# Performance work log

Hardware: AMD Instinct MI355X
Metric: run time of the kernel (lower is better)

Reference implementation:

```python
import jax, jax.numpy as jnp
import numpy as np

B, N, C = 8, 1024, 768
LOCAL_DIM = C // 2      # local_ratio = 0.5
GLOBAL_DIM = C - LOCAL_DIM
HEADS = 12 // 2         # num_heads // div
HEAD_DIM = GLOBAL_DIM // HEADS
SCALE = HEAD_DIM ** -0.5
KS = 3                  # local_ks
HIDDEN = 4 * C
EPS = 1e-6


def setup_inputs() -> dict:
    key = jax.random.key(0)
    ks = jax.random.split(key, 8)
    s = 0.02
    return {
        "x": jax.random.normal(ks[0], (B, N, C), jnp.float32),
        "ln1_g": jnp.ones((GLOBAL_DIM,), jnp.float32),
        "ln1_b": jnp.zeros((GLOBAL_DIM,), jnp.float32),
        "ln1l_g": jnp.ones((LOCAL_DIM,), jnp.float32),
        "ln1l_b": jnp.zeros((LOCAL_DIM,), jnp.float32),
        "g_qkv_w": jax.random.normal(ks[1], (GLOBAL_DIM, 3 * GLOBAL_DIM), jnp.float32) * s,
        "g_proj_w": jax.random.normal(ks[2], (GLOBAL_DIM, GLOBAL_DIM), jnp.float32) * s,
        "g_proj_b": jnp.zeros((GLOBAL_DIM,), jnp.float32),
        "l_qkv_w": jax.random.normal(ks[3], (LOCAL_DIM, 3 * LOCAL_DIM), jnp.float32) * s,
        "l_proj_w": jax.random.normal(ks[4], (LOCAL_DIM, LOCAL_DIM), jnp.float32) * s,
        "l_proj_b": jnp.zeros((LOCAL_DIM,), jnp.float32),
        "ln2_g": jnp.ones((C,), jnp.float32),
        "ln2_b": jnp.zeros((C,), jnp.float32),
        "fc1_w": jax.random.normal(ks[5], (C, HIDDEN), jnp.float32) * s,
        "fc1_b": jnp.zeros((HIDDEN,), jnp.float32),
        "fc2_w": jax.random.normal(ks[6], (HIDDEN, C), jnp.float32) * s,
        "fc2_b": jnp.zeros((C,), jnp.float32),
    }


def _ln(x, g, b):
    m = x.mean(-1, keepdims=True)
    v = x.var(-1, keepdims=True)  # biased, matches torch LayerNorm
    return (x - m) / jnp.sqrt(v + EPS) * g + b


def _mha(x, qkv_w, proj_w, proj_b, band=None):
    b, n, c = x.shape
    qkv = (x @ qkv_w).reshape(b, n, 3, HEADS, c // HEADS)
    q, k, v = qkv[:, :, 0], qkv[:, :, 1], qkv[:, :, 2]  # [b,n,h,d]
    scores = jnp.einsum('bnhd,bmhd->bhnm', q, k) * SCALE
    if band is not None:
        scores = jnp.where(band, scores, -jnp.inf)  # dense band mask, as in source
    a = jax.nn.softmax(scores, axis=-1)
    out = jnp.einsum('bhnm,bmhd->bnhd', a, v).reshape(b, n, c)
    return out @ proj_w + proj_b


def reference(x, ln1_g, ln1_b, ln1l_g, ln1l_b, g_qkv_w, g_proj_w, g_proj_b,
              l_qkv_w, l_proj_w, l_proj_b, ln2_g, ln2_b, fc1_w, fc1_b, fc2_w, fc2_b):
    idx = jnp.arange(N)
    # keep positions |i-j| <= ks//2 (clipping in the torch loop reduces to this band)
    band = (jnp.abs(idx[:, None] - idx[None, :]) <= KS // 2)[None, None]  # [1,1,N,N]
    xg = x[:, :, :GLOBAL_DIM]
    xl = x[:, :, GLOBAL_DIM:]
    attn_out = _mha(_ln(xg, ln1_g, ln1_b), g_qkv_w, g_proj_w, g_proj_b)
    local_out = _mha(_ln(xl, ln1l_g, ln1l_b), l_qkv_w, l_proj_w, l_proj_b, band=band)
    x = x + jnp.concatenate([attn_out, local_out], axis=-1)
    h = _ln(x, ln2_g, ln2_b)
    h = jax.nn.gelu(h @ fc1_w + fc1_b, approximate=False)  # torch default GELU is exact erf
    x = x + (h @ fc2_w + fc2_b)
    return x
```

## Files before the change

kernel.cpp:

```cpp
#include <hip/hip_runtime.h>

#define B_ 8
#define N_ 1024
#define C_ 768
#define H_ 6
#define HID_ 3072
#define EPSV 1e-6f
#define SCALE_V 0.125f
#define DPAD 70

typedef unsigned short u16t;
typedef unsigned int u32t;
typedef __attribute__((ext_vector_type(8))) short bf16x8;
typedef __attribute__((ext_vector_type(4))) float f32x4;

__device__ __forceinline__ float b2f(u16t u) {
  union { u32t i; float f; } c; c.i = ((u32t)u) << 16; return c.f;
}
__device__ __forceinline__ u16t f2b(float f) {
  union { float f; u32t i; } c; c.f = f;
  u32t r = c.i + 0x7FFFu + ((c.i >> 16) & 1u);
  return (u16t)(r >> 16);
}
__device__ __forceinline__ float ldval(const float* p) { return *p; }
__device__ __forceinline__ float ldval(const u16t* p) { return b2f(*p); }

__device__ __forceinline__ float gelu_f(float v) {
  const float u = v * (0.79788456f + 0.0356774081f * v * v);
  const float e = __expf(2.f * u);
  const float th = 1.f - 2.f / (e + 1.f);
  return 0.5f * v * (1.f + th);
}

__device__ __forceinline__ void gl16(const u16t* g, u16t* l) {
  __builtin_amdgcn_global_load_lds(
      (const __attribute__((address_space(1))) unsigned int*)g,
      (__attribute__((address_space(3))) unsigned int*)l, 16, 0, 0);
}

__device__ __forceinline__ int xcd_swz2() {
  const int gx = gridDim.x, gy = gridDim.y;
  const int nwg = gx * gy * gridDim.z;
  const int h = blockIdx.x + gx * (blockIdx.y + gy * blockIdx.z);
  const int nloc = nwg >> 3;
  const int rows = nloc / gx;
  const int xcd = h & 7;
  const int loc = h >> 3;
  const int bxl = loc / rows;
  const int byl = loc - bxl * rows;
  return xcd * nloc + byl * gx + bxl;
}

struct W6 {
  const float* w[6];
  u16t* wt[6];
  int K[6]; int N[6];
  int start[7];
};
__global__ __launch_bounds__(256) void prep_k(
    W6 d,
    const float* __restrict__ x,
    const float* __restrict__ gg, const float* __restrict__ gb,
    const float* __restrict__ lg, const float* __restrict__ lb,
    u16t* __restrict__ og, u16t* __restrict__ ol, int rows)
{
  __shared__ u16t tile[32][40];
  const int bid = blockIdx.x;
  if (bid < d.start[6]) {
    int z = 0;
    while (bid >= d.start[z + 1]) ++z;
    const float* W = d.w[z];
    u16t* Wt = d.wt[z];
    const int K = d.K[z], N = d.N[z];
    const int local = bid - d.start[z];
    const int nb = N >> 5;
    const int n0 = (local % nb) * 32, k0 = (local / nb) * 32;
    const int tx = threadIdx.x & 31, ty = threadIdx.x >> 5;
#pragma unroll
    for (int j = 0; j < 4; ++j) {
      const int k = ty + j * 8;
      tile[k][tx] = f2b(W[(size_t)(k0 + k) * N + n0 + tx]);
    }
    __syncthreads();
#pragma unroll
    for (int j = 0; j < 4; ++j) {
      const int n = ty + j * 8;
      Wt[(size_t)(n0 + n) * K + k0 + tx] = tile[tx][n];
    }
  } else {
    const int wv = threadIdx.x >> 6, lane = threadIdx.x & 63;
    const int row = (bid - d.start[6]) * 4 + wv;
    if (row >= rows) return;
    const float* ip = x + (size_t)row * 768;
    float xs[12];
    float s0 = 0.f, ss0 = 0.f, s1 = 0.f, ss1 = 0.f;
#pragma unroll
    for (int c = 0; c < 6; ++c) {
      float v = ip[c * 64 + lane];
      xs[c] = v; s0 += v; ss0 += v * v;
    }
#pragma unroll
    for (int c = 0; c < 6; ++c) {
      float v = ip[384 + c * 64 + lane];
      xs[6 + c] = v; s1 += v; ss1 += v * v;
    }
#pragma unroll
    for (int o = 32; o > 0; o >>= 1) {
      s0 += __shfl_xor(s0, o, 64); ss0 += __shfl_xor(ss0, o, 64);
      s1 += __shfl_xor(s1, o, 64); ss1 += __shfl_xor(ss1, o, 64);
    }
    const float m0 = s0 / 384.f, m1 = s1 / 384.f;
    const float i0 = 1.f / sqrtf(ss0 / 384.f - m0 * m0 + EPSV);
    const float i1 = 1.f / sqrtf(ss1 / 384.f - m1 * m1 + EPSV);
    u16t* o0 = og + (size_t)row * 384;
    u16t* o1 = ol + (size_t)row * 384;
#pragma unroll
    for (int c = 0; c < 6; ++c) {
      const int i = c * 64 + lane;
      o0[i] = f2b((xs[c] - m0) * i0 * gg[i] + gb[i]);
      o1[i] = f2b((xs[6 + c] - m1) * i1 * lg[i] + lb[i]);
    }
  }
}

__global__ __launch_bounds__(256) void ln2_vec(
    const u16t* __restrict__ in,
    const float* __restrict__ gam, const float* __restrict__ bet,
    u16t* __restrict__ outp, int rows)
{
  const int wv = threadIdx.x >> 6, lane = threadIdx.x & 63;
  const int row = blockIdx.x * 4 + wv;
  if (row >= rows) return;
  const u16t* ip = in + (size_t)row * 768;
  u16t va[8], vb[8];
  *reinterpret_cast<uint4*>(va) = *reinterpret_cast<const uint4*>(ip + lane * 8);
  const bool hasb = lane < 32;
  if (hasb)
    *reinterpret_cast<uint4*>(vb) = *reinterpret_cast<const uint4*>(ip + 512 + lane * 8);
  float xa[8], xb[8];
  float s = 0.f, ss = 0.f;
#pragma unroll
  for (int j = 0; j < 8; ++j) { xa[j] = b2f(va[j]); s += xa[j]; ss += xa[j] * xa[j]; }
  if (hasb) {
#pragma unroll
    for (int j = 0; j < 8; ++j) { xb[j] = b2f(vb[j]); s += xb[j]; ss += xb[j] * xb[j]; }
  }
#pragma unroll
  for (int o = 32; o > 0; o >>= 1) {
    s += __shfl_xor(s, o, 64);
    ss += __shfl_xor(ss, o, 64);
  }
  const float m = s / 768.f;
  const float inv = 1.f / sqrtf(ss / 768.f - m * m + EPSV);
  u16t* op = outp + (size_t)row * 768;
  {
    float4 g0 = *reinterpret_cast<const float4*>(gam + lane * 8);
    float4 g1 = *reinterpret_cast<const float4*>(gam + lane * 8 + 4);
    float4 b0 = *reinterpret_cast<const float4*>(bet + lane * 8);
    float4 b1 = *reinterpret_cast<const float4*>(bet + lane * 8 + 4);
    const float gg[8] = {g0.x, g0.y, g0.z, g0.w, g1.x, g1.y, g1.z, g1.w};
    const float bb[8] = {b0.x, b0.y, b0.z, b0.w, b1.x, b1.y, b1.z, b1.w};
    u16t ot[8];
#pragma unroll
    for (int j = 0; j < 8; ++j) ot[j] = f2b((xa[j] - m) * inv * gg[j] + bb[j]);
    *reinterpret_cast<uint4*>(op + lane * 8) = *reinterpret_cast<uint4*>(ot);
  }
  if (hasb) {
    float4 g0 = *reinterpret_cast<const float4*>(gam + 512 + lane * 8);
    float4 g1 = *reinterpret_cast<const float4*>(gam + 512 + lane * 8 + 4);
    float4 b0 = *reinterpret_cast<const float4*>(bet + 512 + lane * 8);
    float4 b1 = *reinterpret_cast<const float4*>(bet + 512 + lane * 8 + 4);
    const float gg[8] = {g0.x, g0.y, g0.z, g0.w, g1.x, g1.y, g1.z, g1.w};
    const float bb[8] = {b0.x, b0.y, b0.z, b0.w, b1.x, b1.y, b1.z, b1.w};
    u16t ot[8];
#pragma unroll
    for (int j = 0; j < 8; ++j) ot[j] = f2b((xb[j] - m) * inv * gg[j] + bb[j]);
    *reinterpret_cast<uint4*>(op + 512 + lane * 8) = *reinterpret_cast<uint4*>(ot);
  }
}

__global__ __launch_bounds__(256) void gemm_mfma(
    const u16t* __restrict__ A0, const u16t* __restrict__ A1, int lda,
    const u16t* __restrict__ B0, const u16t* __restrict__ B1, int ldb,
    const float* bias0, const float* bias1,
    const void* res0, const void* res1, int ldr, int res_f32,
    void* out0, void* out1, int ldo, int out_f32,
    int K, int act)
{
  __shared__ u16t pool[32768];
  u16t (*As)[64] = reinterpret_cast<u16t(*)[64]>(pool);
  u16t (*Bs)[64] = reinterpret_cast<u16t(*)[64]>(pool + 16384);
  const int gx = gridDim.x, gy = gridDim.y;
  int t0f = xcd_swz2();
  const int bx = t0f % gx;
  const int tmp = t0f / gx;
  const int by = tmp % gy;
  const int z = tmp / gy;

  const u16t* Aw  = z ? A1 : A0;
  const u16t* Btw = z ? B1 : B0;
  const float* bias = z ? bias1 : bias0;
  const void* res = z ? res1 : res0;
  void* outp = z ? out1 : out0;

  const int t = threadIdx.x;
  const int m0 = by * 128, n0 = bx * 128;
  const int wid = t >> 6, lane = t & 63;
  const int wr = wid >> 1, wc = wid & 1;
  const int lrow = lane & 15, lk = lane >> 4;

  const int srow = lane >> 3;
  const int scol = ((lane & 7) ^ srow) << 3;
  const u16t* aSrc = Aw  + (size_t)(m0 + wid * 32 + srow) * lda + scol;
  const u16t* bSrc = Btw + (size_t)(n0 + wid * 32 + srow) * ldb + scol;

  auto stage = [&](int bufi, int kt_) {
    u16t* aD = &As[bufi * 128 + wid * 32][0];
    u16t* bD = &Bs[bufi * 128 + wid * 32][0];
#pragma unroll
    for (int i = 0; i < 4; ++i) {
      gl16(aSrc + (size_t)i * 8 * lda + kt_ * 64, aD + i * 8 * 64);
      gl16(bSrc + (size_t)i * 8 * ldb + kt_ * 64, bD + i * 8 * 64);
    }
  };

  f32x4 acc[4][4];
#pragma unroll
  for (int m = 0; m < 4; ++m)
#pragma unroll
    for (int n = 0; n < 4; ++n) acc[m][n] = (f32x4)(0.f);

  const int nt = K >> 6;
  stage(0, 0);
  for (int kt = 0; kt < nt; ++kt) {
    const int cur = kt & 1;
    if (kt + 1 < nt) {
      stage(cur ^ 1, kt + 1);
      asm volatile("s_waitcnt vmcnt(8)" ::: "memory");
    } else {
      asm volatile("s_waitcnt vmcnt(0)" ::: "memory");
    }
    __builtin_amdgcn_s_barrier();
    __builtin_amdgcn_sched_barrier(0);
#pragma unroll
    for (int kk = 0; kk < 2; ++kk) {
      bf16x8 aF[4], bF[4];
      const int k8 = kk * 4 + lk;
#pragma unroll
      for (int f = 0; f < 4; ++f) {
        const int ar = wr * 64 + f * 16 + lrow;
        aF[f] = *reinterpret_cast<const bf16x8*>(&As[cur * 128 + ar][(k8 ^ (ar & 7)) << 3]);
        const int br = wc * 64 + f * 16 + lrow;
        bF[f] = *reinterpret_cast<const bf16x8*>(&Bs[cur * 128 + br][(k8 ^ (br & 7)) << 3]);
      }
#pragma unroll
      for (int m = 0; m < 4; ++m)
#pragma unroll
        for (int n = 0; n < 4; ++n)
          acc[m][n] = __builtin_amdgcn_mfma_f32_16x16x32_bf16(
              aF[m], bF[n], acc[m][n], 0, 0, 0);
    }
    __builtin_amdgcn_s_barrier();
  }

  const int orow0 = (lane >> 4) * 4;
  const int ocol = lane & 15;
  if (out_f32) {
    float (*Cf)[128] = reinterpret_cast<float(*)[128]>(pool);
    __syncthreads();
#pragma unroll
    for (int m = 0; m < 4; ++m) {
#pragma unroll
      for (int n = 0; n < 4; ++n) {
        const int lc2 = wc * 64 + n * 16 + ocol;
        const int gn = n0 + lc2;
        const float bv = bias ? bias[gn] : 0.f;
#pragma unroll
        for (int i = 0; i < 4; ++i) {
          const int lr = wr * 64 + m * 16 + orow0 + i;
          float v = acc[m][n][i] + bv;
          if (act == 1) v = gelu_f(v);
          if (res) v += res_f32 ? ((const float*)res)[(size_t)(m0 + lr) * ldr + gn]
                                : b2f(((const u16t*)res)[(size_t)(m0 + lr) * ldr + gn]);
          Cf[lr][lc2] = v;
        }
      }
    }
    __syncthreads();
    float* ou = (float*)outp;
#pragma unroll
    for (int j = 0; j < 16; ++j) {
      const int c = j * 256 + t;
      const int r = c >> 5, ch = (c & 31) * 4;
      *reinterpret_cast<float4*>(ou + (size_t)(m0 + r) * ldo + n0 + ch) =
          *reinterpret_cast<const float4*>(&Cf[r][ch]);
    }
  } else {
    u16t (*Cs)[136] = reinterpret_cast<u16t(*)[136]>(pool);
    __syncthreads();
#pragma unroll
    for (int m = 0; m < 4; ++m) {
#pragma unroll
      for (int n = 0; n < 4; ++n) {
        const int lc2 = wc * 64 + n * 16 + ocol;
        const int gn = n0 + lc2;
        const float bv = bias ? bias[gn] : 0.f;
#pragma unroll
        for (int i = 0; i < 4; ++i) {
          const int lr = wr * 64 + m * 16 + orow0 + i;
          float v = acc[m][n][i] + bv;
          if (act == 1) v = gelu_f(v);
          if (res) v += res_f32 ? ((const float*)res)[(size_t)(m0 + lr) * ldr + gn]
                                : b2f(((const u16t*)res)[(size_t)(m0 + lr) * ldr + gn]);
          Cs[lr][lc2] = f2b(v);
        }
      }
    }
    __syncthreads();
    u16t* ou = (u16t*)outp;
#pragma unroll
    for (int j = 0; j < 8; ++j) {
      const int c = j * 256 + t;
      const int r = c >> 4, ch = (c & 15) * 8;
      *reinterpret_cast<uint4*>(ou + (size_t)(m0 + r) * ldo + n0 + ch) =
          *reinterpret_cast<const uint4*>(&Cs[r][ch]);
    }
  }
}

__global__ __launch_bounds__(256) void gemm64_drain(
    const u16t* __restrict__ A, int lda,
    const u16t* __restrict__ Bt, int ldb,
    const float* __restrict__ bias,
    const void* __restrict__ res, int ldr, int res_f32,
    void* __restrict__ outp, int ldo, int out_f32,
    int K, int act)
{
  __shared__ u16t pool[16384];
  u16t (*As)[64] = reinterpret_cast<u16t(*)[64]>(pool);
  u16t (*Bs)[64] = reinterpret_cast<u16t(*)[64]>(pool + 4096);
  const int gx = gridDim.x, gy = gridDim.y;
  int t0f = xcd_swz2();
  const int bx = t0f % gx;
  const int by = (t0f / gx) % gy;

  const int t = threadIdx.x;
  const int m0 = by * 64, n0 = bx * 128;
  const int wid = t >> 6, lane = t & 63;
  const int wr = wid >> 1, wc = wid & 1;
  const int lrow = lane & 15, lk = lane >> 4;

  const int srow = lane >> 3;
  const int scol = ((lane & 7) ^ srow) << 3;
  const u16t* aSrc = A  + (size_t)(m0 + wid * 16 + srow) * lda + scol;
  const u16t* bSrc = Bt + (size_t)(n0 + wid * 32 + srow) * ldb + scol;

  f32x4 acc[2][4];
#pragma unroll
  for (int m = 0; m < 2; ++m)
#pragma unroll
    for (int n = 0; n < 4; ++n) acc[m][n] = (f32x4)(0.f);

  const int nt = K >> 6;
  for (int kt = 0; kt < nt; ++kt) {
    {
      u16t* aD = &As[wid * 16][0];
      u16t* bD = &Bs[wid * 32][0];
#pragma unroll
      for (int i = 0; i < 2; ++i)
        gl16(aSrc + (size_t)i * 8 * lda + kt * 64, aD + i * 8 * 64);
#pragma unroll
      for (int i = 0; i < 4; ++i)
        gl16(bSrc + (size_t)i * 8 * ldb + kt * 64, bD + i * 8 * 64);
    }
    asm volatile("s_waitcnt vmcnt(0)" ::: "memory");
    __builtin_amdgcn_s_barrier();
    __builtin_amdgcn_sched_barrier(0);
#pragma unroll
    for (int kk = 0; kk < 2; ++kk) {
      bf16x8 aF[2], bF[4];
      const int k8 = kk * 4 + lk;
#pragma unroll
      for (int f = 0; f < 2; ++f) {
        const int ar = wr * 32 + f * 16 + lrow;
        aF[f] = *reinterpret_cast<const bf16x8*>(&As[ar][(k8 ^ (ar & 7)) << 3]);
      }
#pragma unroll
      for (int f = 0; f < 4; ++f) {
        const int br = wc * 64 + f * 16 + lrow;
        bF[f] = *reinterpret_cast<const bf16x8*>(&Bs[br][(k8 ^ (br & 7)) << 3]);
      }
#pragma unroll
      for (int m = 0; m < 2; ++m)
#pragma unroll
        for (int n = 0; n < 4; ++n)
          acc[m][n] = __builtin_amdgcn_mfma_f32_16x16x32_bf16(
              aF[m], bF[n], acc[m][n], 0, 0, 0);
    }
    __builtin_amdgcn_s_barrier();
  }

  const int orow0 = (lane >> 4) * 4;
  const int ocol = lane & 15;
  if (out_f32) {
    float (*Cf)[128] = reinterpret_cast<float(*)[128]>(pool);
    __syncthreads();
#pragma unroll
    for (int m = 0; m < 2; ++m) {
#pragma unroll
      for (int n = 0; n < 4; ++n) {
        const int lc2 = wc * 64 + n * 16 + ocol;
        const int gn = n0 + lc2;
        const float bv = bias ? bias[gn] : 0.f;
#pragma unroll
        for (int i = 0; i < 4; ++i) {
          const int lr = wr * 32 + m * 16 + orow0 + i;
          float v = acc[m][n][i] + bv;
          if (act == 1) v = gelu_f(v);
          if (res) v += res_f32 ? ((const float*)res)[(size_t)(m0 + lr) * ldr + gn]
                                : b2f(((const u16t*)res)[(size_t)(m0 + lr) * ldr + gn]);
          Cf[lr][lc2] = v;
        }
      }
    }
    __syncthreads();
    float* ou = (float*)outp;
#pragma unroll
    for (int j = 0; j < 8; ++j) {
      const int c = j * 256 + t;
      const int r = c >> 5, ch = (c & 31) * 4;
      *reinterpret_cast<float4*>(ou + (size_t)(m0 + r) * ldo + n0 + ch) =
          *reinterpret_cast<const float4*>(&Cf[r][ch]);
    }
  } else {
    u16t (*Cs)[136] = reinterpret_cast<u16t(*)[136]>(pool);
    __syncthreads();
#pragma unroll
    for (int m = 0; m < 2; ++m) {
#pragma unroll
      for (int n = 0; n < 4; ++n) {
        const int lc2 = wc * 64 + n * 16 + ocol;
        const int gn = n0 + lc2;
        const float bv = bias ? bias[gn] : 0.f;
#pragma unroll
        for (int i = 0; i < 4; ++i) {
          const int lr = wr * 32 + m * 16 + orow0 + i;
          float v = acc[m][n][i] + bv;
          if (act == 1) v = gelu_f(v);
          if (res) v += res_f32 ? ((const float*)res)[(size_t)(m0 + lr) * ldr + gn]
                                : b2f(((const u16t*)res)[(size_t)(m0 + lr) * ldr + gn]);
          Cs[lr][lc2] = f2b(v);
        }
      }
    }
    __syncthreads();
    u16t* ou = (u16t*)outp;
#pragma unroll
    for (int j = 0; j < 4; ++j) {
      const int c = j * 256 + t;
      const int r = c >> 4, ch = (c & 15) * 8;
      *reinterpret_cast<uint4*>(ou + (size_t)(m0 + r) * ldo + n0 + ch) =
          *reinterpret_cast<const uint4*>(&Cs[r][ch]);
    }
  }
}

__global__ __launch_bounds__(256) void attn_both(
    const u16t* __restrict__ qkvg, const u16t* __restrict__ qkvl,
    u16t* __restrict__ og, u16t* __restrict__ ol)
{
  __shared__ u16t Ks[64][DPAD];
  __shared__ u16t Vt[64][DPAD];
  __shared__ u16t Pw[4][16][DPAD];
  const int t = threadIdx.x;
  const int bid = blockIdx.x;

  if (bid < 768) {
    const int tf = (bid & 7) * 96 + (bid >> 3);
    const int q0 = (tf % 16) * 64;
    const int h = (tf / 16) % H_;
    const int b = tf / (16 * H_);
    const size_t base = (size_t)b * N_ * 1152 + h * 64;

    const int wid = t >> 6, lane = t & 63;
    const int lc = lane & 15;
    const int lg = lane >> 4;

    bf16x8 qf[2];
    {
      const u16t* qp = qkvg + base + (size_t)(q0 + wid * 16 + lc) * 1152 + 8 * lg;
      qf[0] = *reinterpret_cast<const bf16x8*>(qp);
      qf[1] = *reinterpret_cast<const bf16x8*>(qp + 32);
    }

    f32x4 Of[4];
#pragma unroll
    for (int nf = 0; nf < 4; ++nf) Of[nf] = (f32x4)(0.f);
    float m_run[4], l_run[4];
#pragma unroll
    for (int i = 0; i < 4; ++i) { m_run[i] = -INFINITY; l_run[i] = 0.f; }

    const int sj = t >> 2, sd0 = (t & 3) * 16;

    for (int kt = 0; kt < 16; ++kt) {
      __syncthreads();
      {
        const u16t* kp = qkvg + base + (size_t)(kt * 64 + sj) * 1152 + 384 + sd0;
        uint4 k0 = *reinterpret_cast<const uint4*>(kp);
        uint4 k1 = *reinterpret_cast<const uint4*>(kp + 8);
        *reinterpret_cast<uint4*>(&Ks[sj][sd0])     = k0;
        *reinterpret_cast<uint4*>(&Ks[sj][sd0 + 8]) = k1;
        const u16t* vp = kp + 384;
        u16t tv[16];
        *reinterpret_cast<uint4*>(tv)     = *reinterpret_cast<const uint4*>(vp);
        *reinterpret_cast<uint4*>(tv + 8) = *reinterpret_cast<const uint4*>(vp + 8);
#pragma unroll
        for (int e = 0; e < 16; ++e) Vt[sd0 + e][sj] = tv[e];
      }
      __syncthreads();

      f32x4 sc[4];
#pragma unroll
      for (int nf = 0; nf < 4; ++nf) sc[nf] = (f32x4)(0.f);
      __builtin_amdgcn_s_setprio(1);
#pragma unroll
      for (int kc = 0; kc < 2; ++kc) {
#pragma unroll
        for (int nf = 0; nf < 4; ++nf) {
          bf16x8 kf = *reinterpret_cast<const bf16x8*>(&Ks[nf * 16 + lc][8 * lg + 32 * kc]);
          sc[nf] = __builtin_amdgcn_mfma_f32_16x16x32_bf16(qf[kc], kf, sc[nf], 0, 0, 0);
        }
      }
      __builtin_amdgcn_s_setprio(0);

#pragma unroll
      for (int i = 0; i < 4; ++i) {
        float s0 = sc[0][i] * SCALE_V, s1 = sc[1][i] * SCALE_V;
        float s2 = sc[2][i] * SCALE_V, s3 = sc[3][i] * SCALE_V;
        float mi = fmaxf(fmaxf(s0, s1), fmaxf(s2, s3));
#pragma unroll
        for (int o = 8; o > 0; o >>= 1) mi = fmaxf(mi, __shfl_xor(mi, o, 64));
        const float nm = fmaxf(m_run[i], mi);
        const float alpha = __expf(m_run[i] - nm);
        m_run[i] = nm;
        float p0 = __expf(s0 - nm), p1 = __expf(s1 - nm);
        float p2 = __expf(s2 - nm), p3 = __expf(s3 - nm);
        const int prow = lg * 4 + i;
        Pw[wid][prow][lc]      = f2b(p0);
        Pw[wid][prow][16 + lc] = f2b(p1);
        Pw[wid][prow][32 + lc] = f2b(p2);
        Pw[wid][prow][48 + lc] = f2b(p3);
        float ls = p0 + p1 + p2 + p3;
#pragma unroll
        for (int o = 8; o > 0; o >>= 1) ls += __shfl_xor(ls, o, 64);
        l_run[i] = l_run[i] * alpha + ls;
#pragma unroll
        for (int nf = 0; nf < 4; ++nf) Of[nf][i] *= alpha;
      }

      __builtin_amdgcn_s_setprio(1);
#pragma unroll
      for (int kc = 0; kc < 2; ++kc) {
        bf16x8 pf = *reinterpret_cast<const bf16x8*>(&Pw[wid][lc][8 * lg + 32 * kc]);
#pragma unroll
        for (int nf = 0; nf < 4; ++nf) {
          bf16x8 vf = *reinterpret_cast<const bf16x8*>(&Vt[nf * 16 + lc][8 * lg + 32 * kc]);
          Of[nf] = __builtin_amdgcn_mfma_f32_16x16x32_bf16(pf, vf, Of[nf], 0, 0, 0);
        }
      }
      __builtin_amdgcn_s_setprio(0);
    }

#pragma unroll
    for (int i = 0; i < 4; ++i) {
      const float inv = 1.f / l_run[i];
      const size_t row = (size_t)b * N_ + q0 + wid * 16 + lg * 4 + i;
#pragma unroll
      for (int nf = 0; nf < 4; ++nf)
        og[row * 384 + h * 64 + nf * 16 + lc] = f2b(Of[nf][i] * inv);
    }
  } else {
    const int tg = (bid - 768) * 256 + t;
    const int h = tg % H_;
    const int n = (tg / H_) % N_;
    const int b = tg / (H_ * N_);
    const size_t qb = ((size_t)b * N_ + n) * 1152 + h * 64;

    float q[64];
#pragma unroll
    for (int dc = 0; dc < 8; ++dc) {
      u16t tq[8];
      *reinterpret_cast<uint4*>(tq) = *reinterpret_cast<const uint4*>(qkvl + qb + dc * 8);
#pragma unroll
      for (int s2 = 0; s2 < 8; ++s2) q[dc * 8 + s2] = b2f(tq[s2]);
    }

    const int jm = (n > 0) ? n - 1 : 0;
    const int jp = (n < N_ - 1) ? n + 1 : N_ - 1;
    const size_t kb0 = ((size_t)b * N_ + jm) * 1152 + 384 + h * 64;
    const size_t kb1 = ((size_t)b * N_ + n ) * 1152 + 384 + h * 64;
    const size_t kb2 = ((size_t)b * N_ + jp) * 1152 + 384 + h * 64;

    float s0 = 0.f, s1 = 0.f, s2v = 0.f;
#pragma unroll
    for (int dc = 0; dc < 8; ++dc) {
      u16t t0[8], t1[8], t2[8];
      *reinterpret_cast<uint4*>(t0) = *reinterpret_cast<const uint4*>(qkvl + kb0 + dc * 8);
      *reinterpret_cast<uint4*>(t1) = *reinterpret_cast<const uint4*>(qkvl + kb1 + dc * 8);
      *reinterpret_cast<uint4*>(t2) = *reinterpret_cast<const uint4*>(qkvl + kb2 + dc * 8);
#pragma unroll
      for (int s = 0; s < 8; ++s) {
        float qv = q[dc * 8 + s];
        s0 = fmaf(qv, b2f(t0[s]), s0);
        s1 = fmaf(qv, b2f(t1[s]), s1);
        s2v = fmaf(qv, b2f(t2[s]), s2v);
      }
    }
    s0 = (n > 0)      ? s0 * SCALE_V : -1e30f;
    s1 = s1 * SCALE_V;
    s2v = (n < N_ - 1) ? s2v * SCALE_V : -1e30f;
    float m = fmaxf(s1, fmaxf(s0, s2v));
    float p0 = __expf(s0 - m), p1 = __expf(s1 - m), p2 = __expf(s2v - m);
    float inv = 1.f / (p0 + p1 + p2);
    p0 *= inv; p1 *= inv; p2 *= inv;

    const size_t vb0 = kb0 + 384, vb1 = kb1 + 384, vb2 = kb2 + 384;
    u16t* op = ol + ((size_t)b * N_ + n) * 384 + h * 64;
#pragma unroll
    for (int dc = 0; dc < 8; ++dc) {
      u16t t0[8], t1[8], t2[8], ot[8];
      *reinterpret_cast<uint4*>(t0) = *reinterpret_cast<const uint4*>(qkvl + vb0 + dc * 8);
      *reinterpret_cast<uint4*>(t1) = *reinterpret_cast<const uint4*>(qkvl + vb1 + dc * 8);
      *reinterpret_cast<uint4*>(t2) = *reinterpret_cast<const uint4*>(qkvl + vb2 + dc * 8);
#pragma unroll
      for (int s = 0; s < 8; ++s)
        ot[s] = f2b(p0 * b2f(t0[s]) + p1 * b2f(t1[s]) + p2 * b2f(t2[s]));
      *reinterpret_cast<uint4*>(op + dc * 8) = *reinterpret_cast<uint4*>(ot);
    }
  }
}

extern "C" void kernel_launch(void* const* d_in, const int* in_sizes, int n_in,
                              void* d_out, int out_size, void* d_ws, size_t ws_size,
                              hipStream_t stream) {
  const float* x        = (const float*)d_in[0];
  const float* ln1_g    = (const float*)d_in[1];
  const float* ln1_b    = (const float*)d_in[2];
  const float* ln1l_g   = (const float*)d_in[3];
  const float* ln1l_b   = (const float*)d_in[4];
  const float* g_qkv_w  = (const float*)d_in[5];
  const float* g_proj_w = (const float*)d_in[6];
  const float* g_proj_b = (const float*)d_in[7];
  const float* l_qkv_w  = (const float*)d_in[8];
  const float* l_proj_w = (const float*)d_in[9];
  const float* l_proj_b = (const float*)d_in[10];
  const float* ln2_g    = (const float*)d_in[11];
  const float* ln2_b    = (const float*)d_in[12];
  const float* fc1_w    = (const float*)d_in[13];
  const float* fc1_b    = (const float*)d_in[14];
  const float* fc2_w    = (const float*)d_in[15];
  const float* fc2_b    = (const float*)d_in[16];
  float* out = (float*)d_out;
  u16t* ws = (u16t*)d_ws;

  u16t* gqkv_wt = ws + 0;
  u16t* lqkv_wt = ws + 442368;
  u16t* gproj_wt= ws + 884736;
  u16t* lproj_wt= ws + 1032192;
  u16t* fc1_wt  = ws + 1179648;
  u16t* fc2_wt  = ws + 3538944;
  u16t* lng  = ws + 5898240;
  u16t* lnl  = ws + 9043968;
  u16t* qkvg = ws + 12189696;
  u16t* qkvl = ws + 21626880;
  u16t* attg = lng;
  u16t* attl = lnl;
  u16t* x1   = ws + 12189696;
  u16t* ln2o = ws + 5898240;
  u16t* hbuf = ws + 18481152;

  const int rows = B_ * N_;

  W6 w6;
  w6.w[0] = g_qkv_w;  w6.wt[0] = gqkv_wt;  w6.K[0] = 384;  w6.N[0] = 1152;
  w6.w[1] = l_qkv_w;  w6.wt[1] = lqkv_wt;  w6.K[1] = 384;  w6.N[1] = 1152;
  w6.w[2] = g_proj_w; w6.wt[2] = gproj_wt; w6.K[2] = 384;  w6.N[2] = 384;
  w6.w[3] = l_proj_w; w6.wt[3] = lproj_wt; w6.K[3] = 384;  w6.N[3] = 384;
  w6.w[4] = fc1_w;    w6.wt[4] = fc1_wt;   w6.K[4] = 768;  w6.N[4] = 3072;
  w6.w[5] = fc2_w;    w6.wt[5] = fc2_wt;   w6.K[5] = 3072; w6.N[5] = 768;
  int acc0 = 0;
  for (int i = 0; i < 6; ++i) {
    w6.start[i] = acc0;
    acc0 += (w6.N[i] / 32) * (w6.K[i] / 32);
  }
  w6.start[6] = acc0;

  prep_k<<<dim3(acc0 + 2048), 256, 0, stream>>>(
      w6, x, ln1_g, ln1_b, ln1l_g, ln1l_b, lng, lnl, rows);

  gemm_mfma<<<dim3(9, 64, 2), 256, 0, stream>>>(
      lng, lnl, 384, gqkv_wt, lqkv_wt, 384,
      nullptr, nullptr, nullptr, nullptr, 0, 0,
      qkvg, qkvl, 1152, 0, 384, 0);

  attn_both<<<dim3(960), 256, 0, stream>>>(qkvg, qkvl, attg, attl);

  gemm_mfma<<<dim3(3, 64, 2), 256, 0, stream>>>(
      attg, attl, 384, gproj_wt, lproj_wt, 384,
      g_proj_b, l_proj_b, x, x + 384, 768, 1,
      x1, x1 + 384, 768, 0, 384, 0);

  ln2_vec<<<dim3(2048), 256, 0, stream>>>(x1, ln2_g, ln2_b, ln2o, rows);

  gemm_mfma<<<dim3(24, 64, 1), 256, 0, stream>>>(
      ln2o, ln2o, 768, fc1_wt, fc1_wt, 768,
      fc1_b, fc1_b, nullptr, nullptr, 0, 0,
      hbuf, hbuf, 3072, 0, 768, 1);

  gemm64_drain<<<dim3(6, 128), 256, 0, stream>>>(
      hbuf, 3072, fc2_wt, 3072, fc2_b, x1, 768, 0,
      out, 768, 1, 3072, 0);
}
```

Before: 255.6 us.

## Use 64-row single-buffer GEMM for QKV/proj, specialize FC1 kernel

Drops the double-buffered 128x128 generic GEMM. The QKV and projection GEMMs now run through the 64x128 single-buffer drain kernel, extended to take two batched z-slices, which doubles the block count and uses less LDS per block. FC1 gets its own 128x128 single-buffer kernel with bias and GELU hard-coded and half the shared memory. This aims at better occupancy and tail behaviour, but gives up the overlap of global loads with MFMA compute.

Measured after the change: 232.4 us (median of 2 runs). 1.1x faster.

```diff
diff --git a/kernel.cpp b/kernel.cpp
--- a/kernel.cpp
+++ b/kernel.cpp
@@ -179,161 +179,105 @@
   }
 }
 
-__global__ __launch_bounds__(256) void gemm_mfma(
+__global__ __launch_bounds__(256) void gemm128_fc1(
+    const u16t* __restrict__ A, int lda,
+    const u16t* __restrict__ Bt, int ldb,
+    const float* __restrict__ bias,
+    u16t* __restrict__ outp, int ldo, int K)
+{
+  __shared__ u16t pool[17408];
+  u16t (*As)[64] = reinterpret_cast<u16t(*)[64]>(pool);
+  u16t (*Bs)[64] = reinterpret_cast<u16t(*)[64]>(pool + 8192);
+  const int gx = gridDim.x, gy = gridDim.y;
+  int t0f = xcd_swz2();
+  const int bx = t0f % gx;
+  const int by = (t0f / gx) % gy;
+
+  const int t = threadIdx.x;
+  const int m0 = by * 128, n0 = bx * 128;
+  const int wid = t >> 6, lane = t & 63;
+  const int wr = wid >> 1, wc = wid & 1;
+  const int lrow = lane & 15, lk = lane >> 4;
+
+  const int srow = lane >> 3;
+  const int scol = ((lane & 7) ^ srow) << 3;
+  const u16t* aSrc = A  + (size_t)(m0 + wid * 32 + srow) * lda + scol;
+  const u16t* bSrc = Bt + (size_t)(n0 + wid * 32 + srow) * ldb + scol;
+
+  f32x4 acc[4][4];
+#pragma unroll
+  for (int m = 0; m < 4; ++m)
+#pragma unroll
+    for (int n = 0; n < 4; ++n) acc[m][n] = (f32x4)(0.f);
+
+  const int nt = K >> 6;
+  for (int kt = 0; kt < nt; ++kt) {
+    {
+      u16t* aD = &As[wid * 32][0];
+      u16t* bD = &Bs[wid * 32][0];
+#pragma unroll
+      for (int i = 0; i < 4; ++i) {
+        gl16(aSrc + (size_t)i * 8 * lda + kt * 64, aD + i * 8 * 64);
+        gl16(bSrc + (size_t)i * 8 * ldb + kt * 64, bD + i * 8 * 64);
+      }
+    }
+    asm volatile("s_waitcnt vmcnt(0)" ::: "memory");
+    __builtin_amdgcn_s_barrier();
+    __builtin_amdgcn_sched_barrier(0);
+#pragma unroll
+    for (int kk = 0; kk < 2; ++kk) {
+      bf16x8 aF[4], bF[4];
+      const int k8 = kk * 4 + lk;
+#pragma unroll
+      for (int f = 0; f < 4; ++f) {
+        const int ar = wr * 64 + f * 16 + lrow;
+        aF[f] = *reinterpret_cast<const bf16x8*>(&As[ar][(k8 ^ (ar & 7)) << 3]);
+        const int br = wc * 64 + f * 16 + lrow;
+        bF[f] = *reinterpret_cast<const bf16x8*>(&Bs[br][(k8 ^ (br & 7)) << 3]);
+      }
+#pragma unroll
+      for (int m = 0; m < 4; ++m)
+#pragma unroll
+        for (int n = 0; n < 4; ++n)
+          acc[m][n] = __builtin_amdgcn_mfma_f32_16x16x32_bf16(
+              aF[m], bF[n], acc[m][n], 0, 0, 0);
+    }
+    __builtin_amdgcn_s_barrier();
+  }
+
+  const int orow0 = (lane >> 4) * 4;
+  const int ocol = lane & 15;
+  u16t (*Cs)[136] = reinterpret_cast<u16t(*)[136]>(pool);
+  __syncthreads();
+#pragma unroll
+  for (int m = 0; m < 4; ++m) {
+#pragma unroll
+    for (int n = 0; n < 4; ++n) {
+      const int lc2 = wc * 64 + n * 16 + ocol;
+      const float bv = bias[n0 + lc2];
+#pragma unroll
+      for (int i = 0; i < 4; ++i) {
+        const int lr = wr * 64 + m * 16 + orow0 + i;
+        Cs[lr][lc2] = f2b(gelu_f(acc[m][n][i] + bv));
+      }
+    }
+  }
+  __syncthreads();
+#pragma unroll
+  for (int j = 0; j < 8; ++j) {
+    const int c = j * 256 + t;
+    const int r = c >> 4, ch = (c & 15) * 8;
+    *reinterpret_cast<uint4*>(outp + (size_t)(m0 + r) * ldo + n0 + ch) =
+        *reinterpret_cast<const uint4*>(&Cs[r][ch]);
+  }
+}
+
+__global__ __launch_bounds__(256) void gemm64_drain(
     const u16t* __restrict__ A0, const u16t* __restrict__ A1, int lda,
     const u16t* __restrict__ B0, const u16t* __restrict__ B1, int ldb,
     const float* bias0, const float* bias1,
     const void* res0, const void* res1, int ldr, int res_f32,
     void* out0, void* out1, int ldo, int out_f32,
-    int K, int act)
-{
-  __shared__ u16t pool[32768];
-  u16t (*As)[64] = reinterpret_cast<u16t(*)[64]>(pool);
-  u16t (*Bs)[64] = reinterpret_cast<u16t(*)[64]>(pool + 16384);
-  const int gx = gridDim.x, gy = gridDim.y;
-  int t0f = xcd_swz2();
-  const int bx = t0f % gx;
-  const int tmp = t0f / gx;
-  const int by = tmp % gy;
-  const int z = tmp / gy;
-
-  const u16t* Aw  = z ? A1 : A0;
-  const u16t* Btw = z ? B1 : B0;
-  const float* bias = z ? bias1 : bias0;
-  const void* res = z ? res1 : res0;
-  void* outp = z ? out1 : out0;
-
-  const int t = threadIdx.x;
-  const int m0 = by * 128, n0 = bx * 128;
-  const int wid = t >> 6, lane = t & 63;
-  const int wr = wid >> 1, wc = wid & 1;
-  const int lrow = lane & 15, lk = lane >> 4;
-
-  const int srow = lane >> 3;
-  const int scol = ((lane & 7) ^ srow) << 3;
-  const u16t* aSrc = Aw  + (size_t)(m0 + wid * 32 + srow) * lda + scol;
-  const u16t* bSrc = Btw + (size_t)(n0 + wid * 32 + srow) * ldb + scol;
-
-  auto stage = [&](int bufi, int kt_) {
-    u16t* aD = &As[bufi * 128 + wid * 32][0];
-    u16t* bD = &Bs[bufi * 128 + wid * 32][0];
-#pragma unroll
-    for (int i = 0; i < 4; ++i) {
-      gl16(aSrc + (size_t)i * 8 * lda + kt_ * 64, aD + i * 8 * 64);
-      gl16(bSrc + (size_t)i * 8 * ldb + kt_ * 64, bD + i * 8 * 64);
-    }
-  };
-
-  f32x4 acc[4][4];
-#pragma unroll
-  for (int m = 0; m < 4; ++m)
-#pragma unroll
-    for (int n = 0; n < 4; ++n) acc[m][n] = (f32x4)(0.f);
-
-  const int nt = K >> 6;
-  stage(0, 0);
-  for (int kt = 0; kt < nt; ++kt) {
-    const int cur = kt & 1;
-    if (kt + 1 < nt) {
-      stage(cur ^ 1, kt + 1);
-      asm volatile("s_waitcnt vmcnt(8)" ::: "memory");
-    } else {
-      asm volatile("s_waitcnt vmcnt(0)" ::: "memory");
-    }
-    __builtin_amdgcn_s_barrier();
-    __builtin_amdgcn_sched_barrier(0);
-#pragma unroll
-    for (int kk = 0; kk < 2; ++kk) {
-      bf16x8 aF[4], bF[4];
-      const int k8 = kk * 4 + lk;
-#pragma unroll
-      for (int f = 0; f < 4; ++f) {
-        const int ar = wr * 64 + f * 16 + lrow;
-        aF[f] = *reinterpret_cast<const bf16x8*>(&As[cur * 128 + ar][(k8 ^ (ar & 7)) << 3]);
-        const int br = wc * 64 + f * 16 + lrow;
-        bF[f] = *reinterpret_cast<const bf16x8*>(&Bs[cur * 128 + br][(k8 ^ (br & 7)) << 3]);
-      }
-#pragma unroll
-      for (int m = 0; m < 4; ++m)
-#pragma unroll
-        for (int n = 0; n < 4; ++n)
-          acc[m][n] = __builtin_amdgcn_mfma_f32_16x16x32_bf16(
-              aF[m], bF[n], acc[m][n], 0, 0, 0);
-    }
-    __builtin_amdgcn_s_barrier();
-  }
-
-  const int orow0 = (lane >> 4) * 4;
-  const int ocol = lane & 15;
-  if (out_f32) {
-    float (*Cf)[128] = reinterpret_cast<float(*)[128]>(pool);
-    __syncthreads();
-#pragma unroll
-    for (int m = 0; m < 4; ++m) {
-#pragma unroll
-      for (int n = 0; n < 4; ++n) {
-        const int lc2 = wc * 64 + n * 16 + ocol;
-        const int gn = n0 + lc2;
-        const float bv = bias ? bias[gn] : 0.f;
-#pragma unroll
-        for (int i = 0; i < 4; ++i) {
-          const int lr = wr * 64 + m * 16 + orow0 + i;
-          float v = acc[m][n][i] + bv;
-          if (act == 1) v = gelu_f(v);
-          if (res) v += res_f32 ? ((const float*)res)[(size_t)(m0 + lr) * ldr + gn]
-                                : b2f(((const u16t*)res)[(size_t)(m0 + lr) * ldr + gn]);
-          Cf[lr][lc2] = v;
-        }
-      }
-    }
-    __syncthreads();
-    float* ou = (float*)outp;
-#pragma unroll
-    for (int j = 0; j < 16; ++j) {
-      const int c = j * 256 + t;
-      const int r = c >> 5, ch = (c & 31) * 4;
-      *reinterpret_cast<float4*>(ou + (size_t)(m0 + r) * ldo + n0 + ch) =
-          *reinterpret_cast<const float4*>(&Cf[r][ch]);
-    }
-  } else {
-    u16t (*Cs)[136] = reinterpret_cast<u16t(*)[136]>(pool);
-    __syncthreads();
-#pragma unroll
-    for (int m = 0; m < 4; ++m) {
-#pragma unroll
-      for (int n = 0; n < 4; ++n) {
-        const int lc2 = wc * 64 + n * 16 + ocol;
-        const int gn = n0 + lc2;
-        const float bv = bias ? bias[gn] : 0.f;
-#pragma unroll
-        for (int i = 0; i < 4; ++i) {
-          const int lr = wr * 64 + m * 16 + orow0 + i;
-          float v = acc[m][n][i] + bv;
-          if (act == 1) v = gelu_f(v);
-          if (res) v += res_f32 ? ((const float*)res)[(size_t)(m0 + lr) * ldr + gn]
-                                : b2f(((const u16t*)res)[(size_t)(m0 + lr) * ldr + gn]);
-          Cs[lr][lc2] = f2b(v);
-        }
-      }
-    }
-    __syncthreads();
-    u16t* ou = (u16t*)outp;
-#pragma unroll
-    for (int j = 0; j < 8; ++j) {
-      const int c = j * 256 + t;
-      const int r = c >> 4, ch = (c & 15) * 8;
-      *reinterpret_cast<uint4*>(ou + (size_t)(m0 + r) * ldo + n0 + ch) =
-          *reinterpret_cast<const uint4*>(&Cs[r][ch]);
-    }
-  }
-}
-
-__global__ __launch_bounds__(256) void gemm64_drain(
-    const u16t* __restrict__ A, int lda,
-    const u16t* __restrict__ Bt, int ldb,
-    const float* __restrict__ bias,
-    const void* __restrict__ res, int ldr, int res_f32,
-    void* __restrict__ outp, int ldo, int out_f32,
     int K, int act)
 {
   __shared__ u16t pool[16384];
@@ -342,7 +286,15 @@
   const int gx = gridDim.x, gy = gridDim.y;
   int t0f = xcd_swz2();
   const int bx = t0f % gx;
-  const int by = (t0f / gx) % gy;
+  const int tmp = t0f / gx;
+  const int by = tmp % gy;
+  const int z = tmp / gy;
+
+  const u16t* Aw  = z ? A1 : A0;
+  const u16t* Btw = z ? B1 : B0;
+  const float* bias = z ? bias1 : bias0;
+  const void* res = z ? res1 : res0;
+  void* outp = z ? out1 : out0;
 
   const int t = threadIdx.x;
   const int m0 = by * 64, n0 = bx * 128;
@@ -352,8 +304,8 @@
 
   const int srow = lane >> 3;
   const int scol = ((lane & 7) ^ srow) << 3;
-  const u16t* aSrc = A  + (size_t)(m0 + wid * 16 + srow) * lda + scol;
-  const u16t* bSrc = Bt + (size_t)(n0 + wid * 32 + srow) * ldb + scol;
+  const u16t* aSrc = Aw  + (size_t)(m0 + wid * 16 + srow) * lda + scol;
+  const u16t* bSrc = Btw + (size_t)(n0 + wid * 32 + srow) * ldb + scol;
 
   f32x4 acc[2][4];
 #pragma unroll
@@ -698,26 +650,25 @@
   prep_k<<<dim3(acc0 + 2048), 256, 0, stream>>>(
       w6, x, ln1_g, ln1_b, ln1l_g, ln1l_b, lng, lnl, rows);
 
-  gemm_mfma<<<dim3(9, 64, 2), 256, 0, stream>>>(
+  gemm64_drain<<<dim3(9, 128, 2), 256, 0, stream>>>(
       lng, lnl, 384, gqkv_wt, lqkv_wt, 384,
       nullptr, nullptr, nullptr, nullptr, 0, 0,
       qkvg, qkvl, 1152, 0, 384, 0);
 
   attn_both<<<dim3(960), 256, 0, stream>>>(qkvg, qkvl, attg, attl);
 
-  gemm_mfma<<<dim3(3, 64, 2), 256, 0, stream>>>(
+  gemm64_drain<<<dim3(3, 128, 2), 256, 0, stream>>>(
       attg, attl, 384, gproj_wt, lproj_wt, 384,
       g_proj_b, l_proj_b, x, x + 384, 768, 1,
       x1, x1 + 384, 768, 0, 384, 0);
 
   ln2_vec<<<dim3(2048), 256, 0, stream>>>(x1, ln2_g, ln2_b, ln2o, rows);
 
-  gemm_mfma<<<dim3(24, 64, 1), 256, 0, stream>>>(
-      ln2o, ln2o, 768, fc1_wt, fc1_wt, 768,
-      fc1_b, fc1_b, nullptr, nullptr, 0, 0,
-      hbuf, hbuf, 3072, 0, 768, 1);
-
-  gemm64_drain<<<dim3(6, 128), 256, 0, stream>>>(
-      hbuf, 3072, fc2_wt, 3072, fc2_b, x1, 768, 0,
-      out, 768, 1, 3072, 0);
-}
+  gemm128_fc1<<<dim3(24, 64), 256, 0, stream>>>(
+      ln2o, 768, fc1_wt, 768, fc1_b, hbuf, 3072, 768);
+
+  gemm64_drain<<<dim3(6, 128, 1), 256, 0, stream>>>(
+      hbuf, hbuf, 3072, fc2_wt, fc2_wt, 3072,
+      fc2_b, fc2_b, x1, x1, 768, 0,
+      out, out, 768, 1, 3072, 0);
+}
```
